# Kernel optimization log

Measured on AMD Instinct MI355X. Metric: run time of the kernel, lower is better.

## Reference

```python
import jax, jax.numpy as jnp
import numpy as np

N = 512          # N_ROIs (nodes)
E = N * N        # number of edges
V = 6            # number of views (edge_attr dim)
DIMS = [(1, 36), (36, 24), (24, 5)]  # (in, out) per NNConv layer


def _nnconv(x, edge_attr, src, dst, We, be, root, bias, cin, cout):
    # edge MLP: Linear + ReLU -> per-edge weight matrix [E, cin, cout]
    w = jax.nn.relu(edge_attr @ We + be).reshape(-1, cin, cout)
    msg = jnp.einsum('ei,eio->eo', x[src], w)              # gather + per-edge matmul
    s = jax.ops.segment_sum(msg, dst, num_segments=N)      # scatter-sum
    cnt = jax.ops.segment_sum(jnp.ones((msg.shape[0], 1), x.dtype), dst, num_segments=N)
    agg = s / jnp.maximum(cnt, 1.0)                        # mean aggregation
    return agg + x @ root + bias                           # root weight + bias (PyG NNConv)


def setup_inputs() -> dict:
    key = jax.random.key(0)
    ks = jax.random.split(key, 16)
    x = jnp.ones((N, 1), jnp.float32)
    edge_attr = jax.random.uniform(ks[0], (E, V), jnp.float32)
    edge_index = jax.random.randint(ks[1], (2, E), 0, N, dtype=jnp.int32)
    inp = {'x': x, 'edge_attr': edge_attr, 'edge_index': edge_index}
    for l, (cin, cout) in enumerate(DIMS, start=1):
        k = jax.random.split(ks[1 + l], 4)
        inp[f'We{l}'] = jax.random.normal(k[0], (V, cin * cout), jnp.float32) / np.sqrt(V)
        inp[f'be{l}'] = jnp.zeros((cin * cout,), jnp.float32)
        inp[f'root{l}'] = jax.random.normal(k[1], (cin, cout), jnp.float32) / np.sqrt(cin)
        inp[f'b{l}'] = jnp.zeros((cout,), jnp.float32)
    return inp


def reference(x, edge_attr, edge_index,
              We1, be1, root1, b1,
              We2, be2, root2, b2,
              We3, be3, root3, b3):
    src, dst = edge_index[0], edge_index[1]
    h = jax.nn.relu(_nnconv(x, edge_attr, src, dst, We1, be1, root1, b1, *DIMS[0]))
    h = jax.nn.relu(_nnconv(h, edge_attr, src, dst, We2, be2, root2, b2, *DIMS[1]))
    h = jax.nn.relu(_nnconv(h, edge_attr, src, dst, We3, be3, root3, b3, *DIMS[2]))
    # pairwise CBT: sum_k |h_i,k - h_j,k|  ->  [N, N]
    cbt = jnp.sum(jnp.abs(h[:, None, :] - h[None, :, :]), axis=2)
    return cbt
```

## Files before the change

### kernel.cpp

```cpp
#include <hip/hip_runtime.h>
#include <hip/hip_bf16.h>

#define N_NODES 512
#define N_EDGES (512 * 512)
#define NBLK 256
#define EPB (N_EDGES / NBLK)

typedef __attribute__((ext_vector_type(2))) _Float16 half2v;

#if defined(__has_builtin)
#if __has_builtin(__builtin_amdgcn_fdot2)
#define FDOT2(a, b, c) __builtin_amdgcn_fdot2((a), (b), (c), false)
#endif
#endif
#ifndef FDOT2
static __device__ inline float fdot2_asm(half2v a, half2v b, float c) {
    float d;
    asm("v_dot2_f32_f16 %0, %1, %2, %3" : "=v"(d) : "v"(a), "v"(b), "v"(c));
    return d;
}
#define FDOT2(a, b, c) fdot2_asm((a), (b), (c))
#endif

static __device__ inline unsigned pack_h2(float x, float y) {
    union { _Float16 h[2]; unsigned u; } c;
    c.h[0] = (_Float16)x;
    c.h[1] = (_Float16)y;
    return c.u;
}
static __device__ inline half2v bits_h2(int b) {
    union { int i; half2v h; } c;
    c.i = b;
    return c.h;
}

__global__ __launch_bounds__(256) void count_kernel(const int* __restrict__ dst,
                                                    int* __restrict__ bcnt_t,
                                                    float* __restrict__ aggz) {
    __shared__ int h[N_NODES];
    int tid = threadIdx.x;
    int b = blockIdx.x;
    h[tid] = 0;
    h[tid + 256] = 0;
    int gt = b * 256 + tid;
    if (gt < 512 * (36 + 24 + 5)) aggz[gt] = 0.f;
    __syncthreads();
#pragma unroll
    for (int k = 0; k < EPB / 256; k++)
        atomicAdd(&h[dst[b * EPB + k * 256 + tid]], 1);
    __syncthreads();
    bcnt_t[tid * NBLK + b] = h[tid];
    bcnt_t[(tid + 256) * NBLK + b] = h[tid + 256];
}

__global__ __launch_bounds__(NBLK) void colscan_kernel(const int* __restrict__ bcnt_t,
                                                       int* __restrict__ pre,
                                                       int* __restrict__ tot) {
    __shared__ int buf[NBLK];
    int t = blockIdx.x;
    int b = threadIdx.x;
    int v = bcnt_t[t * NBLK + b];
    buf[b] = v;
    __syncthreads();
    for (int d = 1; d < NBLK; d <<= 1) {
        int add = (b >= d) ? buf[b - d] : 0;
        __syncthreads();
        buf[b] += add;
        __syncthreads();
    }
    pre[b * N_NODES + t] = buf[b] - v;
    if (b == NBLK - 1) tot[t] = buf[b];
}

__global__ __launch_bounds__(512) void offs_kernel(const int* __restrict__ tot,
                                                   int* __restrict__ offs) {
    __shared__ int buf[N_NODES];
    int t = threadIdx.x;
    int v = tot[t];
    buf[t] = v;
    __syncthreads();
    for (int d = 1; d < N_NODES; d <<= 1) {
        int add = (t >= d) ? buf[t - d] : 0;
        __syncthreads();
        buf[t] += add;
        __syncthreads();
    }
    offs[t + 1] = buf[t];
    if (t == 0) offs[0] = 0;
}

__global__ __launch_bounds__(256) void scatter_kernel(const int* __restrict__ src,
                                                      const int* __restrict__ dst,
                                                      const float* __restrict__ ea,
                                                      const int* __restrict__ pre,
                                                      const int* __restrict__ offs,
                                                      int4* __restrict__ ed4) {
    __shared__ int lcur[N_NODES];
    int tid = threadIdx.x;
    int b = blockIdx.x;
    lcur[tid] = offs[tid] + pre[b * N_NODES + tid];
    lcur[tid + 256] = offs[tid + 256] + pre[b * N_NODES + tid + 256];
    __syncthreads();
#pragma unroll
    for (int k = 0; k < EPB / 256; k++) {
        int e = b * EPB + k * 256 + tid;
        const float* a = ea + (size_t)e * 6;
        float a0 = a[0], a1 = a[1], a2 = a[2], a3 = a[3], a4 = a[4], a5 = a[5];
        int p = atomicAdd(&lcur[dst[e]], 1);
        int4 r;
        r.x = (int)pack_h2(a0, a1);
        r.y = (int)pack_h2(a2, a3);
        r.z = (int)pack_h2(a4, a5);
        r.w = src[e];
        ed4[p] = r;
    }
}

__global__ __launch_bounds__(256) void nnconv_l1(const float* __restrict__ x,
                                                 const int4* __restrict__ ed4,
                                                 const int* __restrict__ offs,
                                                 const float* __restrict__ We,
                                                 const float* __restrict__ be,
                                                 float* __restrict__ agg) {
    constexpr int G = 2;
    __shared__ float lacc[36];
    const int n = blockIdx.x / G;
    const int g = blockIdx.x % G;
    const int tid = threadIdx.x;
    const int w = tid >> 6;
    const int lane = tid & 63;
    const int es = lane >> 2;
    const int oq = lane & 3;

    half2v wrp[9][3];
    float ber[9], acc[9];
#pragma unroll
    for (int q = 0; q < 9; q++) {
        int o = oq * 9 + q;
        ber[q] = be[o];
        acc[q] = 0.f;
#pragma unroll
        for (int t = 0; t < 3; t++)
            wrp[q][t] = bits_h2((int)pack_h2(We[(2 * t) * 36 + o], We[(2 * t + 1) * 36 + o]));
    }

    const int start = offs[n];
    const int end = offs[n + 1];
    const int len = end - start;
    const int per = (len + G - 1) / G;
    int p0 = start + g * per;
    int p1 = p0 + per;
    if (p0 > end) p0 = end;
    if (p1 > end) p1 = end;

    for (int p = p0 + w * 16; p < p1; p += 64) {
        bool v = (p + es) < p1;
        int4 e = v ? ed4[p + es] : make_int4(0, 0, 0, 0);
        float xv = v ? x[e.w & (N_NODES - 1)] : 0.f;
        half2v e01 = bits_h2(e.x), e23 = bits_h2(e.y), e45 = bits_h2(e.z);
#pragma unroll
        for (int q = 0; q < 9; q++) {
            float z = FDOT2(e45, wrp[q][2],
                    FDOT2(e23, wrp[q][1],
                    FDOT2(e01, wrp[q][0], ber[q])));
            acc[q] = fmaf(xv, fmaxf(z, 0.f), acc[q]);
        }
    }

#pragma unroll
    for (int m = 4; m <= 32; m <<= 1) {
#pragma unroll
        for (int q = 0; q < 9; q++) acc[q] += __shfl_xor(acc[q], m, 64);
    }

    if (tid < 36) lacc[tid] = 0.f;
    __syncthreads();
    if (lane < 4) {
#pragma unroll
        for (int q = 0; q < 9; q++) atomicAdd(&lacc[oq * 9 + q], acc[q]);
    }
    __syncthreads();
    if (tid < 36) atomicAdd(&agg[n * 36 + tid], lacc[tid]);
}

template <int CIN, int COUT, int OG, int BLK, int G>
__global__ __launch_bounds__(BLK) void nnconv_edges(
    const float* __restrict__ hprev,
    const int4* __restrict__ ed4,
    const int* __restrict__ offs,
    const float* __restrict__ We,
    const float* __restrict__ be,
    float* __restrict__ agg)
{
    constexpr int J = CIN * COUT;
    constexpr int OPL = COUT / OG;
    constexpr int A = CIN * OPL;

    const int n = blockIdx.x / G;
    const int g = blockIdx.x % G;
    const int tid = threadIdx.x;
    const bool act = (tid < A);
    const int i = act ? tid / OPL : 0;
    const int og = act ? (tid % OPL) * OG : 0;

    half2v wrp[OG][3];
    float ber[OG], acc[OG];
#pragma unroll
    for (int k = 0; k < OG; k++) {
        acc[k] = 0.f;
        int j = i * COUT + og + k;
        if (act) {
            ber[k] = be[j];
#pragma unroll
            for (int t = 0; t < 3; t++)
                wrp[k][t] = bits_h2((int)pack_h2(We[(2 * t) * J + j], We[(2 * t + 1) * J + j]));
        } else {
            ber[k] = 0.f;
#pragma unroll
            for (int t = 0; t < 3; t++) wrp[k][t] = bits_h2(0);
        }
    }

    const int start = offs[n];
    const int end = offs[n + 1];
    const int len = end - start;
    const int per = (len + G - 1) / G;
    int p = start + g * per;
    int p1 = p + per;
    if (p > end) p = end;
    if (p1 > end) p1 = end;

    const float* hp_i = hprev + i;

    for (; p + 8 <= p1; p += 8) {
        int4 e[8];
#pragma unroll
        for (int u = 0; u < 8; u++) e[u] = ed4[p + u];
        float xg[8];
#pragma unroll
        for (int u = 0; u < 8; u++) xg[u] = hp_i[(e[u].w & (N_NODES - 1)) * CIN];
#pragma unroll
        for (int u = 0; u < 8; u++) {
            half2v e01 = bits_h2(e[u].x), e23 = bits_h2(e[u].y), e45 = bits_h2(e[u].z);
#pragma unroll
            for (int k = 0; k < OG; k++) {
                float z = FDOT2(e45, wrp[k][2],
                        FDOT2(e23, wrp[k][1],
                        FDOT2(e01, wrp[k][0], ber[k])));
                acc[k] = fmaf(xg[u], fmaxf(z, 0.f), acc[k]);
            }
        }
    }
    if (p < p1) {
        int4 e[8];
        float xg[8];
#pragma unroll
        for (int u = 0; u < 8; u++)
            e[u] = (p + u < p1) ? ed4[p + u] : make_int4(0, 0, 0, 0);
#pragma unroll
        for (int u = 0; u < 8; u++)
            xg[u] = (p + u < p1) ? hp_i[(e[u].w & (N_NODES - 1)) * CIN] : 0.f;
#pragma unroll
        for (int u = 0; u < 8; u++) {
            half2v e01 = bits_h2(e[u].x), e23 = bits_h2(e[u].y), e45 = bits_h2(e[u].z);
#pragma unroll
            for (int k = 0; k < OG; k++) {
                float z = FDOT2(e45, wrp[k][2],
                        FDOT2(e23, wrp[k][1],
                        FDOT2(e01, wrp[k][0], ber[k])));
                acc[k] = fmaf(xg[u], fmaxf(z, 0.f), acc[k]);
            }
        }
    }

    __shared__ float lds_acc[J];
    if (act) {
#pragma unroll
        for (int k = 0; k < OG; k++) lds_acc[i * COUT + og + k] = acc[k];
    }
    __syncthreads();
    if (tid < COUT) {
        float sum = 0.f;
#pragma unroll
        for (int ii = 0; ii < CIN; ii++) sum += lds_acc[ii * COUT + tid];
        atomicAdd(&agg[n * COUT + tid], sum);
    }
}

template <int CIN, int COUT>
__global__ __launch_bounds__(64) void nnconv_fin(const float* __restrict__ agg,
                                                 const int* __restrict__ offs,
                                                 const float* __restrict__ hprev,
                                                 const float* __restrict__ root,
                                                 const float* __restrict__ bias,
                                                 float* __restrict__ hout) {
    int n = blockIdx.x;
    int t = threadIdx.x;
    if (t >= COUT) return;
    int cnt = offs[n + 1] - offs[n];
    float inv = 1.f / fmaxf((float)cnt, 1.f);
    float v = agg[n * COUT + t] * inv;
#pragma unroll
    for (int i = 0; i < CIN; i++) v = fmaf(hprev[n * CIN + i], root[i * COUT + t], v);
    v += bias[t];
    hout[n * COUT + t] = fmaxf(v, 0.f);
}

__global__ __launch_bounds__(256) void cbt_kernel(const float* __restrict__ h3,
                                                  float* __restrict__ out) {
    __shared__ float lh[N_NODES * 5];
    int tid = threadIdx.x;
    for (int idx = tid; idx < N_NODES * 5; idx += 256) lh[idx] = h3[idx];
    __syncthreads();
    int i = blockIdx.x;
    float hi[5];
#pragma unroll
    for (int k = 0; k < 5; k++) hi[k] = lh[i * 5 + k];
    for (int j = tid; j < N_NODES; j += 256) {
        float sacc = 0.f;
#pragma unroll
        for (int k = 0; k < 5; k++) sacc += fabsf(hi[k] - lh[j * 5 + k]);
        out[i * N_NODES + j] = sacc;
    }
}

extern "C" void kernel_launch(void* const* d_in, const int* in_sizes, int n_in,
                              void* d_out, int out_size, void* d_ws, size_t ws_size,
                              hipStream_t stream) {
    const float* x = (const float*)d_in[0];
    const float* edge_attr = (const float*)d_in[1];
    const int* edge_index = (const int*)d_in[2];
    const float* We1 = (const float*)d_in[3];
    const float* be1 = (const float*)d_in[4];
    const float* root1 = (const float*)d_in[5];
    const float* b1 = (const float*)d_in[6];
    const float* We2 = (const float*)d_in[7];
    const float* be2 = (const float*)d_in[8];
    const float* root2 = (const float*)d_in[9];
    const float* b2 = (const float*)d_in[10];
    const float* We3 = (const float*)d_in[11];
    const float* be3 = (const float*)d_in[12];
    const float* root3 = (const float*)d_in[13];
    const float* b3 = (const float*)d_in[14];

    const int E = N_EDGES;
    const int* src = edge_index;
    const int* dst = edge_index + E;

    char* ws = (char*)d_ws;
    int* offs = (int*)(ws + 0);
    int* tot = (int*)(ws + 2048);
    int* bcnt_t = (int*)(ws + 4096);
    int* pre = (int*)(ws + 528384);
    int4* ed4 = (int4*)(ws + 1052672);
    float* agg1 = (float*)(ws + 5246976);
    float* agg2 = (float*)(ws + 5320704);
    float* agg3 = (float*)(ws + 5369856);
    float* h1 = (float*)(ws + 5380096);
    float* h2 = (float*)(ws + 5453824);
    float* h3 = (float*)(ws + 5502976);

    count_kernel<<<NBLK, 256, 0, stream>>>(dst, bcnt_t, agg1 );
    colscan_kernel<<<N_NODES, NBLK, 0, stream>>>(bcnt_t, pre, tot);
    offs_kernel<<<1, 512, 0, stream>>>(tot, offs);
    scatter_kernel<<<NBLK, 256, 0, stream>>>(src, dst, edge_attr, pre, offs, ed4);

    nnconv_l1<<<N_NODES * 2, 256, 0, stream>>>(x, ed4, offs, We1, be1, agg1);
    nnconv_fin<1, 36><<<N_NODES, 64, 0, stream>>>(agg1, offs, x, root1, b1, h1);

    nnconv_edges<36, 24, 4, 256, 8><<<N_NODES * 8, 256, 0, stream>>>(h1, ed4, offs, We2, be2, agg2);
    nnconv_fin<36, 24><<<N_NODES, 64, 0, stream>>>(agg2, offs, h1, root2, b2, h2);

    nnconv_edges<24, 5, 1, 128, 8><<<N_NODES * 8, 128, 0, stream>>>(h2, ed4, offs, We3, be3, agg3);
    nnconv_fin<24, 5><<<N_NODES, 64, 0, stream>>>(agg3, offs, h2, root3, b3, h3);

    cbt_kernel<<<N_NODES, 256, 0, stream>>>(h3, (float*)d_out);
}
```

Baseline: 193.3 us.

## Balance edge-conv work with fixed edge ranges per block spanning node boundaries

The layer 2 and 3 edge kernels now give each block a fixed, equal slice of the dst-sorted edge array, in place of a fixed share of each node's edges. Each block stages the CSR offsets in LDS, binary-searches its starting node, and flushes partial sums with an atomic add every time it crosses a node boundary. This is meant to remove load imbalance from uneven node degrees and to reduce the block count. In exchange it adds an offsets copy and a search per block, extra syncs per boundary, and an occupancy hint of 8 in launch_bounds.

Result: slower. 226.7 us (+17.3%).

```diff
diff --git a/kernel.cpp b/kernel.cpp
--- a/kernel.cpp
+++ b/kernel.cpp
@@ -183,8 +183,8 @@
     if (tid < 36) atomicAdd(&agg[n * 36 + tid], lacc[tid]);
 }
 
-template <int CIN, int COUT, int OG, int BLK, int G>
-__global__ __launch_bounds__(BLK) void nnconv_edges(
+template <int CIN, int COUT, int OG, int BLK, int NB>
+__global__ __launch_bounds__(BLK, 8) void nnconv_edges_bal(
     const float* __restrict__ hprev,
     const int4* __restrict__ ed4,
     const int* __restrict__ offs,
@@ -195,10 +195,14 @@
     constexpr int J = CIN * COUT;
     constexpr int OPL = COUT / OG;
     constexpr int A = CIN * OPL;
-
-    const int n = blockIdx.x / G;
-    const int g = blockIdx.x % G;
+    constexpr int EB = N_EDGES / NB;
+
+    __shared__ float lds_acc[J];
+    __shared__ int loffs[N_NODES + 1];
+
     const int tid = threadIdx.x;
+    for (int idx = tid; idx <= N_NODES; idx += BLK) loffs[idx] = offs[idx];
+
     const bool act = (tid < A);
     const int i = act ? tid / OPL : 0;
     const int og = act ? (tid % OPL) * OG : 0;
@@ -220,70 +224,85 @@
             for (int t = 0; t < 3; t++) wrp[k][t] = bits_h2(0);
         }
     }
-
-    const int start = offs[n];
-    const int end = offs[n + 1];
-    const int len = end - start;
-    const int per = (len + G - 1) / G;
-    int p = start + g * per;
-    int p1 = p + per;
-    if (p > end) p = end;
-    if (p1 > end) p1 = end;
+    __syncthreads();
+
+    const int e0 = blockIdx.x * EB;
+    const int e1 = e0 + EB;
+
+    int lo = 0, hi = N_NODES - 1;
+    while (lo < hi) {
+        int mid = (lo + hi + 1) >> 1;
+        if (loffs[mid] <= e0) lo = mid; else hi = mid - 1;
+    }
+    int n0 = lo;
 
     const float* hp_i = hprev + i;
-
-    for (; p + 8 <= p1; p += 8) {
-        int4 e[8];
-#pragma unroll
-        for (int u = 0; u < 8; u++) e[u] = ed4[p + u];
-        float xg[8];
-#pragma unroll
-        for (int u = 0; u < 8; u++) xg[u] = hp_i[(e[u].w & (N_NODES - 1)) * CIN];
-#pragma unroll
-        for (int u = 0; u < 8; u++) {
-            half2v e01 = bits_h2(e[u].x), e23 = bits_h2(e[u].y), e45 = bits_h2(e[u].z);
+    int p = e0;
+    for (;;) {
+        int send = loffs[n0 + 1];
+        if (send > e1) send = e1;
+
+        for (; p + 8 <= send; p += 8) {
+            int4 e[8];
+#pragma unroll
+            for (int u = 0; u < 8; u++) e[u] = ed4[p + u];
+            float xg[8];
+#pragma unroll
+            for (int u = 0; u < 8; u++) xg[u] = hp_i[(e[u].w & (N_NODES - 1)) * CIN];
+#pragma unroll
+            for (int u = 0; u < 8; u++) {
+                half2v e01 = bits_h2(e[u].x), e23 = bits_h2(e[u].y), e45 = bits_h2(e[u].z);
+#pragma unroll
+                for (int k = 0; k < OG; k++) {
+                    float z = FDOT2(e45, wrp[k][2],
+                            FDOT2(e23, wrp[k][1],
+                            FDOT2(e01, wrp[k][0], ber[k])));
+                    acc[k] = fmaf(xg[u], fmaxf(z, 0.f), acc[k]);
+                }
+            }
+        }
+        if (p < send) {
+            int4 e[8];
+            float xg[8];
+#pragma unroll
+            for (int u = 0; u < 8; u++)
+                e[u] = (p + u < send) ? ed4[p + u] : make_int4(0, 0, 0, 0);
+#pragma unroll
+            for (int u = 0; u < 8; u++)
+                xg[u] = (p + u < send) ? hp_i[(e[u].w & (N_NODES - 1)) * CIN] : 0.f;
+#pragma unroll
+            for (int u = 0; u < 8; u++) {
+                half2v e01 = bits_h2(e[u].x), e23 = bits_h2(e[u].y), e45 = bits_h2(e[u].z);
+#pragma unroll
+                for (int k = 0; k < OG; k++) {
+                    float z = FDOT2(e45, wrp[k][2],
+                            FDOT2(e23, wrp[k][1],
+                            FDOT2(e01, wrp[k][0], ber[k])));
+                    acc[k] = fmaf(xg[u], fmaxf(z, 0.f), acc[k]);
+                }
+            }
+            p = send;
+        }
+
+        if (act) {
 #pragma unroll
             for (int k = 0; k < OG; k++) {
-                float z = FDOT2(e45, wrp[k][2],
-                        FDOT2(e23, wrp[k][1],
-                        FDOT2(e01, wrp[k][0], ber[k])));
-                acc[k] = fmaf(xg[u], fmaxf(z, 0.f), acc[k]);
+                lds_acc[i * COUT + og + k] = acc[k];
+                acc[k] = 0.f;
             }
         }
-    }
-    if (p < p1) {
-        int4 e[8];
-        float xg[8];
-#pragma unroll
-        for (int u = 0; u < 8; u++)
-            e[u] = (p + u < p1) ? ed4[p + u] : make_int4(0, 0, 0, 0);
-#pragma unroll
-        for (int u = 0; u < 8; u++)
-            xg[u] = (p + u < p1) ? hp_i[(e[u].w & (N_NODES - 1)) * CIN] : 0.f;
-#pragma unroll
-        for (int u = 0; u < 8; u++) {
-            half2v e01 = bits_h2(e[u].x), e23 = bits_h2(e[u].y), e45 = bits_h2(e[u].z);
-#pragma unroll
-            for (int k = 0; k < OG; k++) {
-                float z = FDOT2(e45, wrp[k][2],
-                        FDOT2(e23, wrp[k][1],
-                        FDOT2(e01, wrp[k][0], ber[k])));
-                acc[k] = fmaf(xg[u], fmaxf(z, 0.f), acc[k]);
-            }
-        }
-    }
-
-    __shared__ float lds_acc[J];
-    if (act) {
-#pragma unroll
-        for (int k = 0; k < OG; k++) lds_acc[i * COUT + og + k] = acc[k];
-    }
-    __syncthreads();
-    if (tid < COUT) {
-        float sum = 0.f;
-#pragma unroll
-        for (int ii = 0; ii < CIN; ii++) sum += lds_acc[ii * COUT + tid];
-        atomicAdd(&agg[n * COUT + tid], sum);
+        __syncthreads();
+        if (tid < COUT) {
+            float sum = 0.f;
+#pragma unroll
+            for (int ii = 0; ii < CIN; ii++) sum += lds_acc[ii * COUT + tid];
+            atomicAdd(&agg[n0 * COUT + tid], sum);
+        }
+        __syncthreads();
+
+        if (p >= e1) break;
+        ++n0;
+        while (loffs[n0 + 1] <= p) ++n0;
     }
 }
 
@@ -368,10 +387,12 @@
     nnconv_l1<<<N_NODES * 2, 256, 0, stream>>>(x, ed4, offs, We1, be1, agg1);
     nnconv_fin<1, 36><<<N_NODES, 64, 0, stream>>>(agg1, offs, x, root1, b1, h1);
 
-    nnconv_edges<36, 24, 4, 256, 8><<<N_NODES * 8, 256, 0, stream>>>(h1, ed4, offs, We2, be2, agg2);
+    nnconv_edges_bal<36, 24, 4, 256, 2048><<<2048, 256, 0, stream>>>(
+        h1, ed4, offs, We2, be2, agg2);
     nnconv_fin<36, 24><<<N_NODES, 64, 0, stream>>>(agg2, offs, h1, root2, b2, h2);
 
-    nnconv_edges<24, 5, 1, 128, 8><<<N_NODES * 8, 128, 0, stream>>>(h2, ed4, offs, We3, be3, agg3);
+    nnconv_edges_bal<24, 5, 1, 128, 4096><<<4096, 128, 0, stream>>>(
+        h2, ed4, offs, We3, be3, agg3);
     nnconv_fin<24, 5><<<N_NODES, 64, 0, stream>>>(agg3, offs, h2, root3, b3, h3);
 
     cbt_kernel<<<N_NODES, 256, 0, stream>>>(h3, (float*)d_out);
```

## Store hidden features transposed and pre-scale source indices into byte offsets

Applied to the files above, without the earlier changes.

Hidden activations h1/h2 are now stored feature-major (transposed), and the scatter kernel stores each source index pre-multiplied by 4 so gathers become a single byte-offset add. This drops the mask and multiply in the inner gather loop, and lanes that share an edge read one feature column. The edge-loop index is made wave-uniform with readfirstlane so the edge records can be loaded through scalar paths. The h1T/h2T buffers are moved into the workspace region formerly used by the prefix array, which relies on that region being dead by then. Dropping the index mask removes a safety bound on src values.

Result: slower. 275.4 us (+42.5%).

```diff
diff --git a/kernel.cpp b/kernel.cpp
--- a/kernel.cpp
+++ b/kernel.cpp
@@ -111,7 +111,7 @@
         r.x = (int)pack_h2(a0, a1);
         r.y = (int)pack_h2(a2, a3);
         r.z = (int)pack_h2(a4, a5);
-        r.w = src[e];
+        r.w = src[e] << 2;
         ed4[p] = r;
     }
 }
@@ -156,7 +156,7 @@
     for (int p = p0 + w * 16; p < p1; p += 64) {
         bool v = (p + es) < p1;
         int4 e = v ? ed4[p + es] : make_int4(0, 0, 0, 0);
-        float xv = v ? x[e.w & (N_NODES - 1)] : 0.f;
+        float xv = v ? *(const float*)((const char*)x + (unsigned)e.w) : 0.f;
         half2v e01 = bits_h2(e.x), e23 = bits_h2(e.y), e45 = bits_h2(e.z);
 #pragma unroll
         for (int q = 0; q < 9; q++) {
@@ -185,7 +185,7 @@
 
 template <int CIN, int COUT, int OG, int BLK, int G>
 __global__ __launch_bounds__(BLK) void nnconv_edges(
-    const float* __restrict__ hprev,
+    const float* __restrict__ hT,
     const int4* __restrict__ ed4,
     const int* __restrict__ offs,
     const float* __restrict__ We,
@@ -202,6 +202,7 @@
     const bool act = (tid < A);
     const int i = act ? tid / OPL : 0;
     const int og = act ? (tid % OPL) * OG : 0;
+    const unsigned ioff = (unsigned)i * (N_NODES * 4);
 
     half2v wrp[OG][3];
     float ber[OG], acc[OG];
@@ -230,15 +231,17 @@
     if (p > end) p = end;
     if (p1 > end) p1 = end;
 
-    const float* hp_i = hprev + i;
+    const char* hb = (const char*)hT;
 
     for (; p + 8 <= p1; p += 8) {
+        int pu = __builtin_amdgcn_readfirstlane(p);
         int4 e[8];
 #pragma unroll
-        for (int u = 0; u < 8; u++) e[u] = ed4[p + u];
+        for (int u = 0; u < 8; u++) e[u] = ed4[pu + u];
         float xg[8];
 #pragma unroll
-        for (int u = 0; u < 8; u++) xg[u] = hp_i[(e[u].w & (N_NODES - 1)) * CIN];
+        for (int u = 0; u < 8; u++)
+            xg[u] = *(const float*)(hb + ((unsigned)e[u].w + ioff));
 #pragma unroll
         for (int u = 0; u < 8; u++) {
             half2v e01 = bits_h2(e[u].x), e23 = bits_h2(e[u].y), e45 = bits_h2(e[u].z);
@@ -252,14 +255,15 @@
         }
     }
     if (p < p1) {
+        int pu = __builtin_amdgcn_readfirstlane(p);
         int4 e[8];
         float xg[8];
 #pragma unroll
         for (int u = 0; u < 8; u++)
-            e[u] = (p + u < p1) ? ed4[p + u] : make_int4(0, 0, 0, 0);
+            e[u] = (p + u < p1) ? ed4[pu + u] : make_int4(0, 0, 0, 0);
 #pragma unroll
         for (int u = 0; u < 8; u++)
-            xg[u] = (p + u < p1) ? hp_i[(e[u].w & (N_NODES - 1)) * CIN] : 0.f;
+            xg[u] = (p + u < p1) ? *(const float*)(hb + ((unsigned)e[u].w + ioff)) : 0.f;
 #pragma unroll
         for (int u = 0; u < 8; u++) {
             half2v e01 = bits_h2(e[u].x), e23 = bits_h2(e[u].y), e45 = bits_h2(e[u].z);
@@ -287,10 +291,10 @@
     }
 }
 
-template <int CIN, int COUT>
+template <int CIN, int COUT, int TOUT>
 __global__ __launch_bounds__(64) void nnconv_fin(const float* __restrict__ agg,
                                                  const int* __restrict__ offs,
-                                                 const float* __restrict__ hprev,
+                                                 const float* __restrict__ hprevT,
                                                  const float* __restrict__ root,
                                                  const float* __restrict__ bias,
                                                  float* __restrict__ hout) {
@@ -301,9 +305,12 @@
     float inv = 1.f / fmaxf((float)cnt, 1.f);
     float v = agg[n * COUT + t] * inv;
 #pragma unroll
-    for (int i = 0; i < CIN; i++) v = fmaf(hprev[n * CIN + i], root[i * COUT + t], v);
+    for (int i = 0; i < CIN; i++)
+        v = fmaf(hprevT[i * N_NODES + n], root[i * COUT + t], v);
     v += bias[t];
-    hout[n * COUT + t] = fmaxf(v, 0.f);
+    v = fmaxf(v, 0.f);
+    if (TOUT) hout[t * N_NODES + n] = v;
+    else hout[n * COUT + t] = v;
 }
 
 __global__ __launch_bounds__(256) void cbt_kernel(const float* __restrict__ h3,
@@ -356,8 +363,8 @@
     float* agg1 = (float*)(ws + 5246976);
     float* agg2 = (float*)(ws + 5320704);
     float* agg3 = (float*)(ws + 5369856);
-    float* h1 = (float*)(ws + 5380096);
-    float* h2 = (float*)(ws + 5453824);
+    float* h1T = (float*)(ws + 528384);
+    float* h2T = (float*)(ws + 602112);
     float* h3 = (float*)(ws + 5502976);
 
     count_kernel<<<NBLK, 256, 0, stream>>>(dst, bcnt_t, agg1 );
@@ -366,13 +373,15 @@
     scatter_kernel<<<NBLK, 256, 0, stream>>>(src, dst, edge_attr, pre, offs, ed4);
 
     nnconv_l1<<<N_NODES * 2, 256, 0, stream>>>(x, ed4, offs, We1, be1, agg1);
-    nnconv_fin<1, 36><<<N_NODES, 64, 0, stream>>>(agg1, offs, x, root1, b1, h1);
-
-    nnconv_edges<36, 24, 4, 256, 8><<<N_NODES * 8, 256, 0, stream>>>(h1, ed4, offs, We2, be2, agg2);
-    nnconv_fin<36, 24><<<N_NODES, 64, 0, stream>>>(agg2, offs, h1, root2, b2, h2);
-
-    nnconv_edges<24, 5, 1, 128, 8><<<N_NODES * 8, 128, 0, stream>>>(h2, ed4, offs, We3, be3, agg3);
-    nnconv_fin<24, 5><<<N_NODES, 64, 0, stream>>>(agg3, offs, h2, root3, b3, h3);
+    nnconv_fin<1, 36, 1><<<N_NODES, 64, 0, stream>>>(agg1, offs, x, root1, b1, h1T);
+
+    nnconv_edges<36, 24, 4, 256, 8><<<N_NODES * 8, 256, 0, stream>>>(
+        h1T, ed4, offs, We2, be2, agg2);
+    nnconv_fin<36, 24, 1><<<N_NODES, 64, 0, stream>>>(agg2, offs, h1T, root2, b2, h2T);
+
+    nnconv_edges<24, 5, 1, 128, 8><<<N_NODES * 8, 128, 0, stream>>>(
+        h2T, ed4, offs, We3, be3, agg3);
+    nnconv_fin<24, 5, 0><<<N_NODES, 64, 0, stream>>>(agg3, offs, h2T, root3, b3, h3);
 
     cbt_kernel<<<N_NODES, 256, 0, stream>>>(h3, (float*)d_out);
 }
```
